# Optimization experiments

Measured on AMD Instinct MI355X. Metric: run time of the kernel, lower is better.

Reference implementation:

```python
import jax, jax.numpy as jnp
import numpy as np

N = 100000      # nodes (cells)
E = 1600000     # edges (kNN graph, avg degree 16)
DIM_IN = 128    # input features per cell
H = 8           # heads
C1 = 8          # per-head channels, layer 1 (concat -> 64)
DIM_OUT = 10    # classes (concat=False -> mean over heads)
NEG_SLOPE = 0.2


def setup_inputs() -> dict:
    key = jax.random.key(0)
    ks = jax.random.split(key, 10)
    s = 0.1
    return {
        "x": jax.random.normal(ks[0], (N, DIM_IN), dtype=jnp.float32),
        "edge_index": jax.random.randint(ks[1], (2, E), 0, N, dtype=jnp.int64),
        "W1": jax.random.normal(ks[2], (DIM_IN, H * C1), dtype=jnp.float32) * s,
        "a_src1": jax.random.normal(ks[3], (H, C1), dtype=jnp.float32) * s,
        "a_dst1": jax.random.normal(ks[4], (H, C1), dtype=jnp.float32) * s,
        "b1": jnp.zeros((H * C1,), dtype=jnp.float32),
        "W2": jax.random.normal(ks[5], (H * C1, H * DIM_OUT), dtype=jnp.float32) * s,
        "a_src2": jax.random.normal(ks[6], (H, DIM_OUT), dtype=jnp.float32) * s,
        "a_dst2": jax.random.normal(ks[7], (H, DIM_OUT), dtype=jnp.float32) * s,
        "b2": jnp.zeros((DIM_OUT,), dtype=jnp.float32),
    }


def _gat_layer(x, src, dst, W, a_src, a_dst, bias, concat, n):
    """PyG-style GATConv: gather -> edge attention -> segment softmax -> scatter."""
    h_, c_ = a_src.shape
    h = (x @ W).reshape(n, h_, c_)                       # [N, H, C]
    alpha_s = jnp.einsum('nhc,hc->nh', h, a_src)         # [N, H]
    alpha_d = jnp.einsum('nhc,hc->nh', h, a_dst)         # [N, H]
    # per-edge logits; PyG: message from src j to dst i, softmax over dst
    e = jax.nn.leaky_relu(alpha_s[src] + alpha_d[dst], NEG_SLOPE)  # [E, H]
    e_max = jax.ops.segment_max(e, dst, num_segments=n)            # [N, H]
    e = jnp.exp(e - e_max[dst])
    denom = jax.ops.segment_sum(e, dst, num_segments=n)            # [N, H]
    alpha = e / denom[dst]                                          # [E, H]
    msg = h[src] * alpha[:, :, None]                                # [E, H, C]
    out = jax.ops.segment_sum(msg, dst, num_segments=n)             # [N, H, C]
    out = out.reshape(n, h_ * c_) if concat else out.mean(axis=1)
    return out + bias


def reference(x, edge_index, W1, a_src1, a_dst1, b1, W2, a_src2, a_dst2, b2):
    n = x.shape[0]
    loops = jnp.arange(n, dtype=edge_index.dtype)
    src = jnp.concatenate([edge_index[0], loops])  # PyG adds self-loops by default
    dst = jnp.concatenate([edge_index[1], loops])
    h = _gat_layer(x, src, dst, W1, a_src1, a_dst1, b1, True, n)   # [N, 64]
    h = jax.nn.elu(h)
    h = _gat_layer(h, src, dst, W2, a_src2, a_dst2, b2, False, n)  # [N, dim_out]
    return jax.nn.log_softmax(h, axis=1)
```

## Files before the change

kernel.cpp:

```cpp
#include <hip/hip_runtime.h>
#include <hip/hip_bf16.h>
#include <cstdint>

#define CAP 64
#define SLICES 8
#define CHUNK_EDGES 2048

__device__ __forceinline__ float lrelu(float v) { return fmaxf(v, 0.2f * v); }

typedef float f32x2 __attribute__((ext_vector_type(2)));
__device__ __forceinline__ int f2q4(float a, float b, float c, float d) {
    int p = __builtin_amdgcn_cvt_pk_fp8_f32(a, b, 0, false);
    p = __builtin_amdgcn_cvt_pk_fp8_f32(c, d, p, true);
    return p;
}
__device__ __forceinline__ float b2f(unsigned short u) { return __uint_as_float(((unsigned)u) << 16); }
__device__ __forceinline__ unsigned short f2b(float f) {
    unsigned u = __float_as_uint(f);
    return (unsigned short)((u + 0x7FFFu + ((u >> 16) & 1u)) >> 16);
}

__global__ __launch_bounds__(256, 4) void k_bg(const int* __restrict__ ei, int E, int N,
                                               int* __restrict__ cnt, int* __restrict__ bucket,
                                               const float* __restrict__ x,
                                               const float* __restrict__ W,
                                               const float* __restrict__ asrc,
                                               const float* __restrict__ adst,
                                               unsigned char* __restrict__ h1q,
                                               float* __restrict__ ald,
                                               int buildBlocks) {
    __shared__ unsigned short xs[64 * 132];
    if ((int)blockIdx.x < buildBlocks) {
        const int s = blockIdx.x & (SLICES - 1);
        const int chunk = blockIdx.x >> 3;
        const int sliceN = (N + SLICES - 1) / SLICES;
        const int lo = s * sliceN;
        const int hi = min(N, lo + sliceN);
        const int base = chunk * CHUNK_EDGES;
        if (base + CHUNK_EDGES <= E) {
            const int e0 = base + (int)threadIdx.x * 4;
            const int e1 = e0 + 1024;
            int4 d0 = *(const int4*)(ei + E + e0);
            int4 s0 = *(const int4*)(ei + e0);
            int4 d1 = *(const int4*)(ei + E + e1);
            int4 s1 = *(const int4*)(ei + e1);
            int a0 = -1, a1 = -1, a2 = -1, a3 = -1, a4 = -1, a5 = -1, a6 = -1, a7 = -1;
            if (d0.x >= lo && d0.x < hi) a0 = atomicAdd(&cnt[d0.x], 1);
            if (d0.y >= lo && d0.y < hi) a1 = atomicAdd(&cnt[d0.y], 1);
            if (d0.z >= lo && d0.z < hi) a2 = atomicAdd(&cnt[d0.z], 1);
            if (d0.w >= lo && d0.w < hi) a3 = atomicAdd(&cnt[d0.w], 1);
            if (d1.x >= lo && d1.x < hi) a4 = atomicAdd(&cnt[d1.x], 1);
            if (d1.y >= lo && d1.y < hi) a5 = atomicAdd(&cnt[d1.y], 1);
            if (d1.z >= lo && d1.z < hi) a6 = atomicAdd(&cnt[d1.z], 1);
            if (d1.w >= lo && d1.w < hi) a7 = atomicAdd(&cnt[d1.w], 1);
            if (a0 >= 0 && a0 < CAP) bucket[(size_t)d0.x * CAP + a0] = s0.x;
            if (a1 >= 0 && a1 < CAP) bucket[(size_t)d0.y * CAP + a1] = s0.y;
            if (a2 >= 0 && a2 < CAP) bucket[(size_t)d0.z * CAP + a2] = s0.z;
            if (a3 >= 0 && a3 < CAP) bucket[(size_t)d0.w * CAP + a3] = s0.w;
            if (a4 >= 0 && a4 < CAP) bucket[(size_t)d1.x * CAP + a4] = s1.x;
            if (a5 >= 0 && a5 < CAP) bucket[(size_t)d1.y * CAP + a5] = s1.y;
            if (a6 >= 0 && a6 < CAP) bucket[(size_t)d1.z * CAP + a6] = s1.z;
            if (a7 >= 0 && a7 < CAP) bucket[(size_t)d1.w * CAP + a7] = s1.w;
        } else {
            const int end = E;
            for (int e = base + (int)threadIdx.x; e < end; e += 256) {
                int d = ei[E + e];
                if (d >= lo && d < hi) {
                    int a = atomicAdd(&cnt[d], 1);
                    if (a < CAP) bucket[(size_t)d * CAP + a] = ei[e];
                }
            }
        }
        return;
    }
    const int t = threadIdx.x;
    const int rowBase = ((int)blockIdx.x - buildBlocks) * 64;
#pragma unroll
    for (int i = 0; i < 8; ++i) {
        int g = i * 256 + t;
        int r = g >> 5, c4 = (g & 31) << 2;
        float4 v = make_float4(0.f, 0.f, 0.f, 0.f);
        int row = rowBase + r;
        if (row < N) v = *(const float4*)(x + (size_t)row * 128 + c4);
        ushort4 u;
        u.x = f2b(v.x); u.y = f2b(v.y); u.z = f2b(v.z); u.w = f2b(v.w);
        *(ushort4*)(&xs[r * 132 + c4]) = u;
    }
    __syncthreads();
    const int tx = t & 15;
    const int ty = t >> 4;
    float acc[4][4] = {};
#pragma unroll 2
    for (int kc = 0; kc < 32; ++kc) {
        float a_[4][4];
#pragma unroll
        for (int i = 0; i < 4; ++i) {
            ushort4 u = *(const ushort4*)(&xs[(4 * ty + i) * 132 + kc * 4]);
            a_[i][0] = b2f(u.x); a_[i][1] = b2f(u.y); a_[i][2] = b2f(u.z); a_[i][3] = b2f(u.w);
        }
        float4 w[4];
#pragma unroll
        for (int kk = 0; kk < 4; ++kk) w[kk] = *(const float4*)(W + (size_t)(kc * 4 + kk) * 64 + tx * 4);
#pragma unroll
        for (int i = 0; i < 4; ++i) {
#pragma unroll
            for (int j = 0; j < 4; ++j) {
                acc[i][j] += a_[i][0] * ((const float*)&w[0])[j]
                           + a_[i][1] * ((const float*)&w[1])[j]
                           + a_[i][2] * ((const float*)&w[2])[j]
                           + a_[i][3] * ((const float*)&w[3])[j];
            }
        }
    }
    const int h = tx >> 1;
    float4 av = *(const float4*)(asrc + tx * 4);
    float4 dv = *(const float4*)(adst + tx * 4);
    __syncthreads();
    unsigned char* qs = (unsigned char*)xs;
#pragma unroll
    for (int i = 0; i < 4; ++i) {
        int row = rowBase + 4 * ty + i;
        float ps = acc[i][0] * av.x + acc[i][1] * av.y + acc[i][2] * av.z + acc[i][3] * av.w;
        float pd = acc[i][0] * dv.x + acc[i][1] * dv.y + acc[i][2] * dv.z + acc[i][3] * dv.w;
        ps += __shfl_xor(ps, 1);
        pd += __shfl_xor(pd, 1);
        *(int*)(qs + (4 * ty + i) * 96 + h * 12 + (tx & 1) * 4) =
            f2q4(acc[i][0], acc[i][1], acc[i][2], acc[i][3]);
        if ((tx & 1) == 0) {
            *(unsigned short*)(qs + (4 * ty + i) * 96 + h * 12 + 8) = f2b(ps);
            if (row < N) ald[(size_t)row * 8 + h] = pd;
        }
    }
    __syncthreads();
    for (int g = t; g < 1536; g += 256) {
        int row = g / 24;
        if (rowBase + row < N)
            *(unsigned int*)(h1q + (size_t)rowBase * 96 + (size_t)g * 4) = ((unsigned int*)qs)[g];
    }
}

__global__ __launch_bounds__(256) void k_ag(const int* __restrict__ cnt, const int* __restrict__ bucket,
                                            const unsigned char* __restrict__ h1q,
                                            const float* __restrict__ aldin,
                                            const float* __restrict__ b1,
                                            const float* __restrict__ W,
                                            const float* __restrict__ asrc,
                                            const float* __restrict__ adst,
                                            unsigned char* __restrict__ h2q,
                                            float* __restrict__ ald, int N) {
    __shared__ unsigned short xs[32 * 68];
    __shared__ unsigned short wt[80 * 68];
    const int t = threadIdx.x;
    const int rowBase = blockIdx.x * 32;
#pragma unroll
    for (int i = 0; i < 20; ++i) {
        int g = i * 256 + t;
        int k = g / 80, c = g % 80;
        wt[c * 68 + k] = f2b(W[g]);
    }
    {
        const int nl = t >> 3;
        const int h = t & 7;
        const int n = rowBase + nl;
        if (n < N) {
            const float aldh = aldin[(size_t)n * 8 + h];
            float acc[8] = {};
            float den = 0.f;
            auto body = [&](int m0, int m1, int m2, float val) {
                float a_s = b2f((unsigned short)(m2 & 0xFFFF));
                float wl = __expf(lrelu(a_s + aldh)) * val;
                den += wl;
                f32x2 v;
                v = __builtin_amdgcn_cvt_pk_f32_fp8(m0, false); acc[0] += wl * v.x; acc[1] += wl * v.y;
                v = __builtin_amdgcn_cvt_pk_f32_fp8(m0, true);  acc[2] += wl * v.x; acc[3] += wl * v.y;
                v = __builtin_amdgcn_cvt_pk_f32_fp8(m1, false); acc[4] += wl * v.x; acc[5] += wl * v.y;
                v = __builtin_amdgcn_cvt_pk_f32_fp8(m1, true);  acc[6] += wl * v.x; acc[7] += wl * v.y;
            };
            {
                const unsigned char* r = h1q + (size_t)n * 96 + h * 12;
                body(*(const int*)r, *(const int*)(r + 4), *(const int*)(r + 8), 1.f);
            }
            const int k = min(cnt[n], CAP);
            const int* bp = bucket + (size_t)n * CAP;
            if (k > 0) {
                const int kg4 = ((k - 1) >> 2) << 2;
                int4 lo = *(const int4*)(bp);
                int4 hi = *(const int4*)(bp + min(4, kg4));
                for (int i0 = 0; i0 < k; i0 += 8) {
                    int4 cA = lo, cB = hi;
                    lo = *(const int4*)(bp + min(i0 + 8, kg4));
                    hi = *(const int4*)(bp + min(i0 + 12, kg4));
                    const int rem = k - i0;
                    int s[8];
                    s[0] = cA.x;
                    s[1] = (rem > 1) ? cA.y : cA.x;
                    s[2] = (rem > 2) ? cA.z : cA.x;
                    s[3] = (rem > 3) ? cA.w : cA.x;
                    s[4] = (rem > 4) ? cB.x : cA.x;
                    s[5] = (rem > 5) ? cB.y : cA.x;
                    s[6] = (rem > 6) ? cB.z : cA.x;
                    s[7] = (rem > 7) ? cB.w : cA.x;
                    int m0[8], m1[8], m2[8];
#pragma unroll
                    for (int j = 0; j < 8; ++j) {
                        const unsigned char* p = h1q + (size_t)s[j] * 96 + h * 12;
                        m0[j] = *(const int*)p;
                        m1[j] = *(const int*)(p + 4);
                        m2[j] = *(const int*)(p + 8);
                    }
#pragma unroll
                    for (int j = 0; j < 8; ++j) body(m0[j], m1[j], m2[j], (rem > j) ? 1.f : 0.f);
                }
            }
            float inv = 1.f / den;
            float o[8];
#pragma unroll
            for (int j = 0; j < 8; ++j) {
                float v = acc[j] * inv + b1[h * 8 + j];
                o[j] = v > 0.f ? v : __expf(v) - 1.f;
            }
            unsigned short* dst = &xs[nl * 68 + h * 8];
            ushort4 u0, u1;
            u0.x = f2b(o[0]); u0.y = f2b(o[1]); u0.z = f2b(o[2]); u0.w = f2b(o[3]);
            u1.x = f2b(o[4]); u1.y = f2b(o[5]); u1.z = f2b(o[6]); u1.w = f2b(o[7]);
            *(ushort4*)(dst) = u0;
            *(ushort4*)(dst + 4) = u1;
        }
    }
    __syncthreads();
    const int tx = t & 15;
    const int ty = t >> 4;
    float acc[2][5] = {};
#pragma unroll 4
    for (int kc = 0; kc < 16; ++kc) {
        float4 a[2];
#pragma unroll
        for (int i = 0; i < 2; ++i) {
            ushort4 u = *(const ushort4*)(&xs[(2 * ty + i) * 68 + kc * 4]);
            a[i] = make_float4(b2f(u.x), b2f(u.y), b2f(u.z), b2f(u.w));
        }
        float4 w[5];
#pragma unroll
        for (int j = 0; j < 5; ++j) {
            ushort4 u = *(const ushort4*)(&wt[(5 * tx + j) * 68 + kc * 4]);
            w[j] = make_float4(b2f(u.x), b2f(u.y), b2f(u.z), b2f(u.w));
        }
#pragma unroll
        for (int i = 0; i < 2; ++i) {
#pragma unroll
            for (int j = 0; j < 5; ++j) {
                acc[i][j] += a[i].x * w[j].x + a[i].y * w[j].y + a[i].z * w[j].z + a[i].w * w[j].w;
            }
        }
    }
    const int h = tx >> 1;
    float a2[5], d2[5];
#pragma unroll
    for (int j = 0; j < 5; ++j) { a2[j] = asrc[tx * 5 + j]; d2[j] = adst[tx * 5 + j]; }
    __syncthreads();
    unsigned char* qs = (unsigned char*)xs;
#pragma unroll
    for (int i = 0; i < 2; ++i) {
        int row = rowBase + 2 * ty + i;
        float ps = 0.f, pd = 0.f;
#pragma unroll
        for (int j = 0; j < 5; ++j) { ps += acc[i][j] * a2[j]; pd += acc[i][j] * d2[j]; }
        ps += __shfl_xor(ps, 1);
        pd += __shfl_xor(pd, 1);
        int p0 = __builtin_amdgcn_cvt_pk_fp8_f32(acc[i][0], acc[i][1], 0, false);
        int p1 = __builtin_amdgcn_cvt_pk_fp8_f32(acc[i][2], acc[i][3], 0, false);
        int p2 = __builtin_amdgcn_cvt_pk_fp8_f32(acc[i][4], acc[i][4], 0, false);
        unsigned char* q = qs + (2 * ty + i) * 96 + h * 12 + (tx & 1) * 5;
        q[0] = (unsigned char)(p0 & 0xFF);
        q[1] = (unsigned char)((p0 >> 8) & 0xFF);
        q[2] = (unsigned char)(p1 & 0xFF);
        q[3] = (unsigned char)((p1 >> 8) & 0xFF);
        q[4] = (unsigned char)(p2 & 0xFF);
        if ((tx & 1) == 0) {
            *(unsigned short*)(qs + (size_t)(2 * ty + i) * 96 + h * 12 + 10) = f2b(ps);
            if (row < N) ald[(size_t)row * 8 + h] = pd;
        }
    }
    __syncthreads();
    for (int g = t; g < 768; g += 256) {
        int row = g / 24;
        if (rowBase + row < N)
            *(unsigned int*)(h2q + (size_t)rowBase * 96 + (size_t)g * 4) = ((unsigned int*)qs)[g];
    }
}

__global__ __launch_bounds__(256) void k_agg2(const int* __restrict__ cnt, const int* __restrict__ bucket,
                                              const unsigned char* __restrict__ h2q,
                                              const float* __restrict__ ald,
                                              const float* __restrict__ b2,
                                              float* __restrict__ out, int N) {
    const int t = threadIdx.x;
    const int n = blockIdx.x * 32 + (t >> 3);
    const int h = t & 7;
    if (n >= N) return;
    float acc[10] = {};
    float den = 0.f;
    const float aldh = ald[(size_t)n * 8 + h];
    auto body = [&](int m0, int m1, int m2, float val) {
        float a_s = b2f((unsigned short)(((unsigned)m2) >> 16));
        float wl = __expf(lrelu(a_s + aldh)) * val;
        den += wl;
        f32x2 v;
        v = __builtin_amdgcn_cvt_pk_f32_fp8(m0, false); acc[0] += wl * v.x; acc[1] += wl * v.y;
        v = __builtin_amdgcn_cvt_pk_f32_fp8(m0, true);  acc[2] += wl * v.x; acc[3] += wl * v.y;
        v = __builtin_amdgcn_cvt_pk_f32_fp8(m1, false); acc[4] += wl * v.x; acc[5] += wl * v.y;
        v = __builtin_amdgcn_cvt_pk_f32_fp8(m1, true);  acc[6] += wl * v.x; acc[7] += wl * v.y;
        v = __builtin_amdgcn_cvt_pk_f32_fp8(m2, false); acc[8] += wl * v.x; acc[9] += wl * v.y;
    };
    {
        const unsigned char* r = h2q + (size_t)n * 96 + h * 12;
        body(*(const int*)r, *(const int*)(r + 4), *(const int*)(r + 8), 1.f);
    }
    const int k = min(cnt[n], CAP);
    const int* bp = bucket + (size_t)n * CAP;
    if (k > 0) {
        const int kg4 = ((k - 1) >> 2) << 2;
        int4 lo = *(const int4*)(bp);
        int4 hi = *(const int4*)(bp + min(4, kg4));
        for (int i0 = 0; i0 < k; i0 += 8) {
            int4 cA = lo, cB = hi;
            lo = *(const int4*)(bp + min(i0 + 8, kg4));
            hi = *(const int4*)(bp + min(i0 + 12, kg4));
            const int rem = k - i0;
            int s[8];
            s[0] = cA.x;
            s[1] = (rem > 1) ? cA.y : cA.x;
            s[2] = (rem > 2) ? cA.z : cA.x;
            s[3] = (rem > 3) ? cA.w : cA.x;
            s[4] = (rem > 4) ? cB.x : cA.x;
            s[5] = (rem > 5) ? cB.y : cA.x;
            s[6] = (rem > 6) ? cB.z : cA.x;
            s[7] = (rem > 7) ? cB.w : cA.x;
            int m0[8], m1[8], m2[8];
#pragma unroll
            for (int j = 0; j < 8; ++j) {
                const unsigned char* p = h2q + (size_t)s[j] * 96 + h * 12;
                m0[j] = *(const int*)p;
                m1[j] = *(const int*)(p + 4);
                m2[j] = *(const int*)(p + 8);
            }
#pragma unroll
            for (int j = 0; j < 8; ++j) body(m0[j], m1[j], m2[j], (rem > j) ? 1.f : 0.f);
        }
    }
    float inv = 1.f / den;
#pragma unroll
    for (int j = 0; j < 10; ++j) acc[j] *= inv;
#pragma unroll
    for (int off = 1; off < 8; off <<= 1) {
#pragma unroll
        for (int j = 0; j < 10; ++j) acc[j] += __shfl_xor(acc[j], off);
    }
    if (h == 0) {
        float m[10];
#pragma unroll
        for (int j = 0; j < 10; ++j) m[j] = acc[j] * 0.125f + b2[j];
        float mx = -1e30f;
#pragma unroll
        for (int j = 0; j < 10; ++j) mx = fmaxf(mx, m[j]);
        float ssum = 0.f;
#pragma unroll
        for (int j = 0; j < 10; ++j) ssum += __expf(m[j] - mx);
        float lg = __logf(ssum);
#pragma unroll
        for (int j = 0; j < 10; ++j) out[(size_t)n * 10 + j] = m[j] - mx - lg;
    }
}

extern "C" void kernel_launch(void* const* d_in, const int* in_sizes, int n_in,
                              void* d_out, int out_size, void* d_ws, size_t ws_size,
                              hipStream_t stream) {
    const float* x     = (const float*)d_in[0];
    const int*   ei    = (const int*)d_in[1];
    const float* W1    = (const float*)d_in[2];
    const float* asrc1 = (const float*)d_in[3];
    const float* adst1 = (const float*)d_in[4];
    const float* b1    = (const float*)d_in[5];
    const float* W2    = (const float*)d_in[6];
    const float* asrc2 = (const float*)d_in[7];
    const float* adst2 = (const float*)d_in[8];
    const float* b2    = (const float*)d_in[9];
    float* out = (float*)d_out;

    int N = in_sizes[0] / 128;
    int E = in_sizes[1] / 2;

    char* base = (char*)d_ws;
    size_t off = 0;
    auto alloc = [&](size_t bytes) {
        char* p = base + off;
        off = (off + bytes + 255) & ~(size_t)255;
        return p;
    };
    int*            cnt    = (int*)alloc((size_t)N * 4);
    int*            bucket = (int*)alloc((size_t)N * CAP * 4);
    unsigned char*  h1q    = (unsigned char*)alloc((size_t)N * 96);
    unsigned char*  h2q    = (unsigned char*)alloc((size_t)N * 96);
    float*          ald    = (float*)alloc((size_t)N * 8 * 4);
    (void)ws_size; (void)n_in; (void)out_size;

    (void)hipMemsetAsync(cnt, 0, (size_t)N * 4, stream);
    int chunks = (E + CHUNK_EDGES - 1) / CHUNK_EDGES;
    int buildBlocks = chunks * SLICES;
    int gemmBlocks = (N + 63) / 64;
    k_bg<<<buildBlocks + gemmBlocks, 256, 0, stream>>>(ei, E, N, cnt, bucket,
                                                       x, W1, asrc1, adst1, h1q, ald, buildBlocks);
    k_ag<<<(N + 31) / 32, 256, 0, stream>>>(cnt, bucket, h1q, ald, b1,
                                            W2, asrc2, adst2, h2q, ald, N);
    k_agg2<<<(N + 31) / 32, 256, 0, stream>>>(cnt, bucket, h2q, ald, b2, out, N);
}
```

Baseline: 298.4 us.

## Split layer-1 node records into packed fp8 features and separate bf16 source-attention array

Layer-1 per-node data moves from a 96-byte padded record (features plus the attention scalar) to a dense 64-byte fp8 feature array and a separate 16-byte bf16 array of source attention logits. The aim is to shrink the bytes the gather in the aggregation kernel touches per neighbor. The adjacency bucket capacity also drops from 64 to 48, which cuts bucket memory but risks truncating high-degree nodes. In exchange each neighbor gather now issues an extra scattered 2-byte load.

```diff
diff --git a/kernel.cpp b/kernel.cpp
--- a/kernel.cpp
+++ b/kernel.cpp
@@ -2,7 +2,7 @@
 #include <hip/hip_bf16.h>
 #include <cstdint>
 
-#define CAP 64
+#define CAP 48
 #define SLICES 8
 #define CHUNK_EDGES 2048
 
@@ -26,7 +26,8 @@
                                                const float* __restrict__ W,
                                                const float* __restrict__ asrc,
                                                const float* __restrict__ adst,
-                                               unsigned char* __restrict__ h1q,
+                                               unsigned char* __restrict__ h1feat,
+                                               unsigned short* __restrict__ als16,
                                                float* __restrict__ ald,
                                                int buildBlocks) {
     __shared__ unsigned short xs[64 * 132];
@@ -117,6 +118,7 @@
     float4 dv = *(const float4*)(adst + tx * 4);
     __syncthreads();
     unsigned char* qs = (unsigned char*)xs;
+    unsigned short* as_st = xs + 2048;
 #pragma unroll
     for (int i = 0; i < 4; ++i) {
         int row = rowBase + 4 * ty + i;
@@ -124,23 +126,36 @@
         float pd = acc[i][0] * dv.x + acc[i][1] * dv.y + acc[i][2] * dv.z + acc[i][3] * dv.w;
         ps += __shfl_xor(ps, 1);
         pd += __shfl_xor(pd, 1);
-        *(int*)(qs + (4 * ty + i) * 96 + h * 12 + (tx & 1) * 4) =
+        *(int*)(qs + (4 * ty + i) * 64 + h * 8 + (tx & 1) * 4) =
             f2q4(acc[i][0], acc[i][1], acc[i][2], acc[i][3]);
         if ((tx & 1) == 0) {
-            *(unsigned short*)(qs + (4 * ty + i) * 96 + h * 12 + 8) = f2b(ps);
+            as_st[(4 * ty + i) * 8 + h] = f2b(ps);
             if (row < N) ald[(size_t)row * 8 + h] = pd;
         }
     }
     __syncthreads();
-    for (int g = t; g < 1536; g += 256) {
-        int row = g / 24;
-        if (rowBase + row < N)
-            *(unsigned int*)(h1q + (size_t)rowBase * 96 + (size_t)g * 4) = ((unsigned int*)qs)[g];
+    {
+        unsigned int* qsu = (unsigned int*)xs;
+        for (int g = t; g < 1024; g += 256) {
+            int row = g >> 4;
+            if (rowBase + row < N)
+                *(unsigned int*)(h1feat + (size_t)rowBase * 64 + (size_t)g * 4) = qsu[g];
+        }
+        unsigned int* asu = (unsigned int*)as_st;
+        if (t < 256) {
+            int g = t;
+            if (g < 256) {
+                int row = g >> 2;
+                if (rowBase + row < N)
+                    *(unsigned int*)((unsigned char*)als16 + (size_t)rowBase * 16 + (size_t)g * 4) = asu[g];
+            }
+        }
     }
 }
 
 __global__ __launch_bounds__(256) void k_ag(const int* __restrict__ cnt, const int* __restrict__ bucket,
-                                            const unsigned char* __restrict__ h1q,
+                                            const unsigned char* __restrict__ h1feat,
+                                            const unsigned short* __restrict__ als16,
                                             const float* __restrict__ aldin,
                                             const float* __restrict__ b1,
                                             const float* __restrict__ W,
@@ -166,8 +181,7 @@
             const float aldh = aldin[(size_t)n * 8 + h];
             float acc[8] = {};
             float den = 0.f;
-            auto body = [&](int m0, int m1, int m2, float val) {
-                float a_s = b2f((unsigned short)(m2 & 0xFFFF));
+            auto body = [&](int m0, int m1, float a_s, float val) {
                 float wl = __expf(lrelu(a_s + aldh)) * val;
                 den += wl;
                 f32x2 v;
@@ -177,8 +191,8 @@
                 v = __builtin_amdgcn_cvt_pk_f32_fp8(m1, true);  acc[6] += wl * v.x; acc[7] += wl * v.y;
             };
             {
-                const unsigned char* r = h1q + (size_t)n * 96 + h * 12;
-                body(*(const int*)r, *(const int*)(r + 4), *(const int*)(r + 8), 1.f);
+                const unsigned char* r = h1feat + (size_t)n * 64 + h * 8;
+                body(*(const int*)r, *(const int*)(r + 4), b2f(als16[(size_t)n * 8 + h]), 1.f);
             }
             const int k = min(cnt[n], CAP);
             const int* bp = bucket + (size_t)n * CAP;
@@ -200,16 +214,17 @@
                     s[5] = (rem > 5) ? cB.y : cA.x;
                     s[6] = (rem > 6) ? cB.z : cA.x;
                     s[7] = (rem > 7) ? cB.w : cA.x;
-                    int m0[8], m1[8], m2[8];
+                    int m0[8], m1[8];
+                    float as[8];
 #pragma unroll
                     for (int j = 0; j < 8; ++j) {
-                        const unsigned char* p = h1q + (size_t)s[j] * 96 + h * 12;
+                        const unsigned char* p = h1feat + (size_t)s[j] * 64 + h * 8;
                         m0[j] = *(const int*)p;
                         m1[j] = *(const int*)(p + 4);
-                        m2[j] = *(const int*)(p + 8);
+                        as[j] = b2f(als16[(size_t)s[j] * 8 + h]);
                     }
 #pragma unroll
-                    for (int j = 0; j < 8; ++j) body(m0[j], m1[j], m2[j], (rem > j) ? 1.f : 0.f);
+                    for (int j = 0; j < 8; ++j) body(m0[j], m1[j], as[j], (rem > j) ? 1.f : 0.f);
                 }
             }
             float inv = 1.f / den;
@@ -397,11 +412,12 @@
         off = (off + bytes + 255) & ~(size_t)255;
         return p;
     };
-    int*            cnt    = (int*)alloc((size_t)N * 4);
-    int*            bucket = (int*)alloc((size_t)N * CAP * 4);
-    unsigned char*  h1q    = (unsigned char*)alloc((size_t)N * 96);
-    unsigned char*  h2q    = (unsigned char*)alloc((size_t)N * 96);
-    float*          ald    = (float*)alloc((size_t)N * 8 * 4);
+    int*             cnt    = (int*)alloc((size_t)N * 4);
+    int*             bucket = (int*)alloc((size_t)N * CAP * 4);
+    unsigned char*   h1feat = (unsigned char*)alloc((size_t)N * 64);
+    unsigned short*  als16  = (unsigned short*)alloc((size_t)N * 8 * 2);
+    unsigned char*   h2q    = (unsigned char*)alloc((size_t)N * 96);
+    float*           ald    = (float*)alloc((size_t)N * 8 * 4);
     (void)ws_size; (void)n_in; (void)out_size;
 
     (void)hipMemsetAsync(cnt, 0, (size_t)N * 4, stream);
@@ -409,8 +425,8 @@
     int buildBlocks = chunks * SLICES;
     int gemmBlocks = (N + 63) / 64;
     k_bg<<<buildBlocks + gemmBlocks, 256, 0, stream>>>(ei, E, N, cnt, bucket,
-                                                       x, W1, asrc1, adst1, h1q, ald, buildBlocks);
-    k_ag<<<(N + 31) / 32, 256, 0, stream>>>(cnt, bucket, h1q, ald, b1,
+                                                       x, W1, asrc1, adst1, h1feat, als16, ald, buildBlocks);
+    k_ag<<<(N + 31) / 32, 256, 0, stream>>>(cnt, bucket, h1feat, als16, ald, b1,
                                             W2, asrc2, adst2, h2q, ald, N);
     k_agg2<<<(N + 31) / 32, 256, 0, stream>>>(cnt, bucket, h2q, ald, b2, out, N);
 }
```

Measured after the change: 301.5 us. Within noise of the previous version (+1.0%).
